# Performance work log

Measured on AMD Instinct MI355X. Metric: run time of the kernel, lower is better.

Reference implementation:

```python
import math
import jax, jax.numpy as jnp
import numpy as np

IN_DIM = 128
OUT_DIM = 128
D_TIME = 64
N_SRC = 50000
N_DST = 50000
E = 800000
SCALE = math.sqrt(2 * OUT_DIM + D_TIME)  # sqrt(attn_input_dim)


def setup_inputs() -> dict:
    key = jax.random.key(0)
    k1, k2, k3, k4, k5, k6, k7 = jax.random.split(key, 7)
    h_src = jax.random.normal(k1, (N_SRC, IN_DIM), dtype=jnp.float32)
    h_dst = jax.random.normal(k2, (N_DST, IN_DIM), dtype=jnp.float32)
    edge_index = jax.random.randint(k3, (2, E), 0, N_DST, dtype=jnp.int32)
    phi_dt = jax.random.normal(k4, (E, D_TIME), dtype=jnp.float32)
    # parameters (Kaiming-ish scaling like nn.Linear defaults)
    W_src = jax.random.normal(k5, (OUT_DIM, IN_DIM), dtype=jnp.float32) / math.sqrt(IN_DIM)
    W_dst = jax.random.normal(k6, (OUT_DIM, IN_DIM), dtype=jnp.float32) / math.sqrt(IN_DIM)
    attn_w = jax.random.normal(k7, (2 * OUT_DIM + D_TIME,), dtype=jnp.float32) / math.sqrt(2 * OUT_DIM + D_TIME)
    return {"h_src": h_src, "h_dst": h_dst, "edge_index": edge_index,
            "phi_dt": phi_dt, "W_src": W_src, "W_dst": W_dst, "attn_w": attn_w}


def reference(h_src, h_dst, edge_index, phi_dt, W_src, W_dst, attn_w):
    num_dst = h_dst.shape[0]
    src_idx, dst_idx = edge_index[0], edge_index[1]
    # gather + per-edge linear projections: [E, out_dim]
    z_s = h_src[src_idx] @ W_src.T
    z_d = h_dst[dst_idx] @ W_dst.T
    # attn(cat([z_s, z_d, phi])) == z_s@a_s + z_d@a_d + phi@a_t (avoids concat)
    a_s = attn_w[:OUT_DIM]
    a_d = attn_w[OUT_DIM:2 * OUT_DIM]
    a_t = attn_w[2 * OUT_DIM:]
    e = z_s @ a_s + z_d @ a_d + phi_dt @ a_t  # [E]
    e = jax.nn.leaky_relu(e, 0.2) / SCALE
    # numerically stable segment softmax over dst neighbourhoods
    seg_max = jax.ops.segment_max(e, dst_idx, num_segments=num_dst)
    ex = jnp.exp(e - seg_max[dst_idx])
    seg_sum = jax.ops.segment_sum(ex, dst_idx, num_segments=num_dst)
    alpha = ex / (seg_sum[dst_idx] + 1e-12)
    # dropout is identity at inference
    msg = alpha[:, None] * z_s  # [E, out_dim]
    out = jax.ops.segment_sum(msg, dst_idx, num_segments=num_dst)  # [N_dst, out_dim]
    return out
```

## Files before the change

### kernel.cpp

```cpp
#include <hip/hip_runtime.h>
#include <hip/hip_fp16.h>
#include <math.h>

#define IN_DIM   128
#define OUT_DIM  128
#define D_TIME   64
#define NSRC     50000
#define NDST     50000
#define NE       800000
#define NPB      20
#define SLOTS    64
#define EPB      256
#define INV_SCALE 0.05590169943749474f

__global__ __launch_bounds__(256) void k_prevec(const float* __restrict__ Ws,
                                                const float* __restrict__ Wd,
                                                const float* __restrict__ attn,
                                                float* __restrict__ v_s,
                                                float* __restrict__ v_d){
    int wv = threadIdx.x >> 6, lane = threadIdx.x & 63;
    int o = blockIdx.x * 4 + wv;
    const float* W = (o < 128) ? Ws : Wd;
    const float* a = (o < 128) ? attn : attn + OUT_DIM;
    float*       v = (o < 128) ? v_s : v_d;
    int k = o & 127;
    int j = 2 * lane;
    float acc = W[(size_t)j*IN_DIM + k] * a[j] + W[(size_t)(j+1)*IN_DIM + k] * a[j+1];
    #pragma unroll
    for (int off = 32; off > 0; off >>= 1) acc += __shfl_down(acc, off, 64);
    if (lane == 0) v[k] = acc;
}

__global__ __launch_bounds__(256, 4) void k_front(const float* __restrict__ h_src,
                                                  const float* __restrict__ h_dst,
                                                  const float* __restrict__ W,
                                                  const float* __restrict__ v_s,
                                                  const float* __restrict__ v_d,
                                                  __half* __restrict__ Zh,
                                                  float* __restrict__ s_src,
                                                  float* __restrict__ s_dst,
                                                  int* __restrict__ counts){
    int t = threadIdx.x;
    if (blockIdx.x < NSRC/NPB){
        __shared__ float hbuf[2][IN_DIM];
        int r  = t >> 1;
        int kh = t & 1;
        float4 wreg[16];
        const float4* wvp = (const float4*)(W + (size_t)r * IN_DIM + kh * 64);
        #pragma unroll
        for (int i = 0; i < 16; ++i) wreg[i] = wvp[i];
        int base = blockIdx.x * NPB;
        if (t < IN_DIM) hbuf[0][t] = h_src[(size_t)base*IN_DIM + t];
        for (int nn = 0; nn < NPB; ++nn){
            __syncthreads();
            if (nn + 1 < NPB && t < IN_DIM)
                hbuf[(nn+1)&1][t] = h_src[(size_t)(base+nn+1)*IN_DIM + t];
            const float* hc = hbuf[nn&1] + kh*64;
            float acc = 0.f;
            #pragma unroll
            for (int i = 0; i < 16; ++i){
                float4 w = wreg[i]; int k = i*4;
                acc += hc[k+0]*w.x + hc[k+1]*w.y + hc[k+2]*w.z + hc[k+3]*w.w;
            }
            acc += __shfl_xor(acc, 1, 64);
            if (!kh) Zh[(size_t)(base+nn)*OUT_DIM + r] = __float2half_rn(acc);
        }
    } else {
        __shared__ float vd[IN_DIM];
        int b = blockIdx.x - NSRC/NPB;
        bool isDst = (b >= NSRC/4);
        const float* h = isDst ? h_dst : h_src;
        const float* v = isDst ? v_d  : v_s;
        float*       s = isDst ? s_dst : s_src;
        int bb = isDst ? (b - NSRC/4) : b;
        if (t < IN_DIM) vd[t] = v[t];
        __syncthreads();
        int wave = t >> 6, lane = t & 63;
        int node = bb * 4 + wave;
        float2 u = ((const float2*)(h + (size_t)node*IN_DIM))[lane];
        float acc = u.x*vd[2*lane] + u.y*vd[2*lane+1];
        #pragma unroll
        for (int off = 32; off > 0; off >>= 1) acc += __shfl_down(acc, off, 64);
        if (lane == 0){
            s[node] = acc;
            if (isDst) counts[node] = 0;
        }
    }
}

__global__ __launch_bounds__(256) void k_edge(const float* __restrict__ phi,
                                              const float* __restrict__ attn,
                                              const int* __restrict__ ei,
                                              const float* __restrict__ s_src,
                                              const float* __restrict__ s_dst,
                                              int2* __restrict__ slots,
                                              int* __restrict__ counts){
    __shared__ float at[D_TIME];
    __shared__ float pts[EPB];
    int t = threadIdx.x;
    if (t < D_TIME) at[t] = attn[2*OUT_DIM + t];
    __syncthreads();
    int sub = t & 15, g = t >> 4;
    int e0 = blockIdx.x * EPB + g;
    float a0 = at[sub*4+0], a1 = at[sub*4+1], a2 = at[sub*4+2], a3 = at[sub*4+3];
    #pragma unroll
    for (int pp = 0; pp < 16; pp += 4){
        float4 w[4];
        #pragma unroll
        for (int q = 0; q < 4; ++q)
            w[q] = ((const float4*)(phi + (size_t)(e0 + (pp+q)*16) * D_TIME))[sub];
        #pragma unroll
        for (int q = 0; q < 4; ++q){
            float acc = w[q].x*a0 + w[q].y*a1 + w[q].z*a2 + w[q].w*a3;
            #pragma unroll
            for (int off = 8; off > 0; off >>= 1) acc += __shfl_xor(acc, off, 64);
            if (sub == 0) pts[g + (pp+q)*16] = acc;
        }
    }
    __syncthreads();
    int e = blockIdx.x * EPB + t;
    int src = ei[e], dst = ei[NE + e];
    float v = s_src[src] + s_dst[dst] + pts[t];
    v = (v > 0.f) ? v : 0.2f * v;
    v *= INV_SCALE;
    int k = atomicAdd(&counts[dst], 1);
    if (k < SLOTS) slots[(dst << 6) + k] = make_int2(src, __float_as_int(v));
}

__global__ __launch_bounds__(256) void k_agg(const int* __restrict__ counts,
                                             const int2* __restrict__ slots,
                                             const __half* __restrict__ Zh,
                                             float* __restrict__ out){
    int wv = threadIdx.x >> 6, lane = threadIdx.x & 63;
    int d = blockIdx.x * 4 + wv;
    int cnt = counts[d]; cnt = (cnt > SLOTS) ? SLOTS : cnt;
    float e = -1e30f; int src = 0;
    if (lane < cnt){
        int2 s = slots[(d << 6) + lane];
        src = s.x; e = __int_as_float(s.y);
    }
    float m = e;
    #pragma unroll
    for (int off = 32; off > 0; off >>= 1) m = fmaxf(m, __shfl_xor(m, off, 64));
    float ex = (lane < cnt) ? __expf(e - m) : 0.f;
    float sum = ex;
    #pragma unroll
    for (int off = 32; off > 0; off >>= 1) sum += __shfl_xor(sum, off, 64);
    float alpha = ex / (sum + 1e-12f);
    float2 acc = make_float2(0.f, 0.f);
    int jmax = (cnt + 7) & ~7;
    for (int j = 0; j < jmax; j += 8){
        float a[8]; int s[8];
        #pragma unroll
        for (int q = 0; q < 8; ++q){
            a[q] = __shfl(alpha, j+q, 64);
            s[q] = __shfl(src,   j+q, 64);
        }
        __half2 z[8];
        #pragma unroll
        for (int q = 0; q < 8; ++q)
            z[q] = ((const __half2*)(Zh + (size_t)s[q] * OUT_DIM))[lane];
        #pragma unroll
        for (int q = 0; q < 8; ++q){
            float2 f = __half22float2(z[q]);
            acc.x += a[q]*f.x;
            acc.y += a[q]*f.y;
        }
    }
    ((float2*)(out + (size_t)d * OUT_DIM))[lane] = acc;
}

extern "C" void kernel_launch(void* const* d_in, const int* in_sizes, int n_in,
                              void* d_out, int out_size, void* d_ws, size_t ws_size,
                              hipStream_t stream){
    const float* h_src = (const float*)d_in[0];
    const float* h_dst = (const float*)d_in[1];
    const int*   ei    = (const int*)d_in[2];
    const float* phi   = (const float*)d_in[3];
    const float* Wsrc  = (const float*)d_in[4];
    const float* Wdst  = (const float*)d_in[5];
    const float* attn  = (const float*)d_in[6];
    float* out = (float*)d_out;

    char* p = (char*)d_ws;
    auto alloc = [&](size_t bytes)->char*{
        char* r = p; p += (bytes + 255) / 256 * 256; return r;
    };
    __half* Zh   = (__half*)alloc((size_t)NSRC*OUT_DIM*2);
    float* s_src = (float*)alloc((size_t)NSRC*4);
    float* s_dst = (float*)alloc((size_t)NDST*4);
    float* v_s   = (float*)alloc(128*4);
    float* v_d   = (float*)alloc(128*4);
    int2*  slots = (int2*)alloc((size_t)NDST*SLOTS*8);
    int*   counts= (int*)alloc((size_t)NDST*4);

    k_prevec<<<64, 256, 0, stream>>>(Wsrc, Wdst, attn, v_s, v_d);
    k_front<<<NSRC/NPB + (NSRC + NDST)/4, 256, 0, stream>>>(
        h_src, h_dst, Wsrc, v_s, v_d, Zh, s_src, s_dst, counts);
    k_edge<<<NE/EPB, 256, 0, stream>>>(phi, attn, ei, s_src, s_dst, slots, counts);
    k_agg<<<NDST/4, 256, 0, stream>>>(counts, slots, Zh, out);
}
```

Before: 463.3 us.

## Fuse src score into projection, batch rows, widen gathers in aggregation

Computes s_src directly from the projected Z rows inside the src projection blocks, so the separate h_src reread and v_s precompute are dropped. The projection now processes four rows per sync round with 40 nodes per block, and dst scoring handles 16 nodes per block. The edge kernel issues 8 phi loads at a time, and aggregation has each half-wave gather different edges with 8-byte loads, then combines the halves with a shuffle. This trades extra shuffle reductions and register pressure for less redundant memory traffic and fewer barriers.

```diff
diff --git a/kernel.cpp b/kernel.cpp
--- a/kernel.cpp
+++ b/kernel.cpp
@@ -8,33 +8,31 @@
 #define NSRC     50000
 #define NDST     50000
 #define NE       800000
-#define NPB      20
+#define NPB      40
+#define GR       4
+#define NR       (NPB/GR)
+#define DPB      16
 #define SLOTS    64
 #define EPB      256
 #define INV_SCALE 0.05590169943749474f
 
-__global__ __launch_bounds__(256) void k_prevec(const float* __restrict__ Ws,
-                                                const float* __restrict__ Wd,
+__global__ __launch_bounds__(256) void k_prevec(const float* __restrict__ Wd,
                                                 const float* __restrict__ attn,
-                                                float* __restrict__ v_s,
                                                 float* __restrict__ v_d){
     int wv = threadIdx.x >> 6, lane = threadIdx.x & 63;
-    int o = blockIdx.x * 4 + wv;
-    const float* W = (o < 128) ? Ws : Wd;
-    const float* a = (o < 128) ? attn : attn + OUT_DIM;
-    float*       v = (o < 128) ? v_s : v_d;
-    int k = o & 127;
+    int k = blockIdx.x * 4 + wv;
     int j = 2 * lane;
-    float acc = W[(size_t)j*IN_DIM + k] * a[j] + W[(size_t)(j+1)*IN_DIM + k] * a[j+1];
+    float acc = Wd[(size_t)j*IN_DIM + k] * attn[OUT_DIM + j]
+              + Wd[(size_t)(j+1)*IN_DIM + k] * attn[OUT_DIM + j + 1];
     #pragma unroll
     for (int off = 32; off > 0; off >>= 1) acc += __shfl_down(acc, off, 64);
-    if (lane == 0) v[k] = acc;
+    if (lane == 0) v_d[k] = acc;
 }
 
 __global__ __launch_bounds__(256, 4) void k_front(const float* __restrict__ h_src,
                                                   const float* __restrict__ h_dst,
                                                   const float* __restrict__ W,
-                                                  const float* __restrict__ v_s,
+                                                  const float* __restrict__ attn,
                                                   const float* __restrict__ v_d,
                                                   __half* __restrict__ Zh,
                                                   float* __restrict__ s_src,
@@ -42,48 +40,73 @@
                                                   int* __restrict__ counts){
     int t = threadIdx.x;
     if (blockIdx.x < NSRC/NPB){
-        __shared__ float hbuf[2][IN_DIM];
+        __shared__ float hbuf[2][GR][IN_DIM];
+        __shared__ float sred[2][4][GR];
         int r  = t >> 1;
         int kh = t & 1;
+        int wv = t >> 6, lane = t & 63;
+        float a_r = attn[r];
         float4 wreg[16];
         const float4* wvp = (const float4*)(W + (size_t)r * IN_DIM + kh * 64);
         #pragma unroll
         for (int i = 0; i < 16; ++i) wreg[i] = wvp[i];
         int base = blockIdx.x * NPB;
-        if (t < IN_DIM) hbuf[0][t] = h_src[(size_t)base*IN_DIM + t];
-        for (int nn = 0; nn < NPB; ++nn){
+        ((float2*)hbuf[0][wv])[lane] =
+            ((const float2*)(h_src + (size_t)(base + wv)*IN_DIM))[lane];
+        for (int rnd = 0; rnd < NR; ++rnd){
             __syncthreads();
-            if (nn + 1 < NPB && t < IN_DIM)
-                hbuf[(nn+1)&1][t] = h_src[(size_t)(base+nn+1)*IN_DIM + t];
-            const float* hc = hbuf[nn&1] + kh*64;
-            float acc = 0.f;
+            if (rnd + 1 < NR)
+                ((float2*)hbuf[(rnd+1)&1][wv])[lane] =
+                    ((const float2*)(h_src + (size_t)(base + (rnd+1)*GR + wv)*IN_DIM))[lane];
+            if (rnd > 0 && t < GR){
+                int pb = (rnd-1)&1;
+                s_src[base + (rnd-1)*GR + t] =
+                    0.5f*(sred[pb][0][t]+sred[pb][1][t]+sred[pb][2][t]+sred[pb][3][t]);
+            }
             #pragma unroll
-            for (int i = 0; i < 16; ++i){
-                float4 w = wreg[i]; int k = i*4;
-                acc += hc[k+0]*w.x + hc[k+1]*w.y + hc[k+2]*w.z + hc[k+3]*w.w;
+            for (int g = 0; g < GR; ++g){
+                const float* hc = hbuf[rnd&1][g] + kh*64;
+                float acc = 0.f;
+                #pragma unroll
+                for (int i = 0; i < 16; ++i){
+                    float4 w = wreg[i]; int k = i*4;
+                    acc += hc[k+0]*w.x + hc[k+1]*w.y + hc[k+2]*w.z + hc[k+3]*w.w;
+                }
+                acc += __shfl_xor(acc, 1, 64);
+                if (!kh) Zh[(size_t)(base+rnd*GR+g)*OUT_DIM + r] = __float2half_rn(acc);
+                float c = acc * a_r;
+                #pragma unroll
+                for (int off = 32; off > 0; off >>= 1) c += __shfl_xor(c, off, 64);
+                if (lane == 0) sred[rnd&1][wv][g] = c;
             }
-            acc += __shfl_xor(acc, 1, 64);
-            if (!kh) Zh[(size_t)(base+nn)*OUT_DIM + r] = __float2half_rn(acc);
+        }
+        __syncthreads();
+        if (t < GR){
+            int pb = (NR-1)&1;
+            s_src[base + (NR-1)*GR + t] =
+                0.5f*(sred[pb][0][t]+sred[pb][1][t]+sred[pb][2][t]+sred[pb][3][t]);
         }
     } else {
         __shared__ float vd[IN_DIM];
         int b = blockIdx.x - NSRC/NPB;
-        bool isDst = (b >= NSRC/4);
-        const float* h = isDst ? h_dst : h_src;
-        const float* v = isDst ? v_d  : v_s;
-        float*       s = isDst ? s_dst : s_src;
-        int bb = isDst ? (b - NSRC/4) : b;
-        if (t < IN_DIM) vd[t] = v[t];
+        if (t < IN_DIM) vd[t] = v_d[t];
         __syncthreads();
-        int wave = t >> 6, lane = t & 63;
-        int node = bb * 4 + wave;
-        float2 u = ((const float2*)(h + (size_t)node*IN_DIM))[lane];
-        float acc = u.x*vd[2*lane] + u.y*vd[2*lane+1];
-        #pragma unroll
-        for (int off = 32; off > 0; off >>= 1) acc += __shfl_down(acc, off, 64);
-        if (lane == 0){
-            s[node] = acc;
-            if (isDst) counts[node] = 0;
+        int wv = t >> 6, lane = t & 63;
+        float v0 = vd[2*lane], v1 = vd[2*lane+1];
+        int n0 = b * DPB + wv;
+        float2 u[4];
+        #pragma unroll
+        for (int it = 0; it < 4; ++it)
+            u[it] = ((const float2*)(h_dst + (size_t)(n0 + it*4)*IN_DIM))[lane];
+        #pragma unroll
+        for (int it = 0; it < 4; ++it){
+            float acc = u[it].x*v0 + u[it].y*v1;
+            #pragma unroll
+            for (int off = 32; off > 0; off >>= 1) acc += __shfl_down(acc, off, 64);
+            if (lane == 0){
+                s_dst[n0 + it*4] = acc;
+                counts[n0 + it*4] = 0;
+            }
         }
     }
 }
@@ -104,13 +127,13 @@
     int e0 = blockIdx.x * EPB + g;
     float a0 = at[sub*4+0], a1 = at[sub*4+1], a2 = at[sub*4+2], a3 = at[sub*4+3];
     #pragma unroll
-    for (int pp = 0; pp < 16; pp += 4){
-        float4 w[4];
-        #pragma unroll
-        for (int q = 0; q < 4; ++q)
+    for (int pp = 0; pp < 16; pp += 8){
+        float4 w[8];
+        #pragma unroll
+        for (int q = 0; q < 8; ++q)
             w[q] = ((const float4*)(phi + (size_t)(e0 + (pp+q)*16) * D_TIME))[sub];
         #pragma unroll
-        for (int q = 0; q < 4; ++q){
+        for (int q = 0; q < 8; ++q){
             float acc = w[q].x*a0 + w[q].y*a1 + w[q].z*a2 + w[q].w*a3;
             #pragma unroll
             for (int off = 8; off > 0; off >>= 1) acc += __shfl_xor(acc, off, 64);
@@ -132,6 +155,7 @@
                                              const __half* __restrict__ Zh,
                                              float* __restrict__ out){
     int wv = threadIdx.x >> 6, lane = threadIdx.x & 63;
+    int half = lane >> 5, sl = lane & 31;
     int d = blockIdx.x * 4 + wv;
     int cnt = counts[d]; cnt = (cnt > SLOTS) ? SLOTS : cnt;
     float e = -1e30f; int src = 0;
@@ -147,27 +171,35 @@
     #pragma unroll
     for (int off = 32; off > 0; off >>= 1) sum += __shfl_xor(sum, off, 64);
     float alpha = ex / (sum + 1e-12f);
-    float2 acc = make_float2(0.f, 0.f);
+    float4 acc4 = make_float4(0.f, 0.f, 0.f, 0.f);
     int jmax = (cnt + 7) & ~7;
     for (int j = 0; j < jmax; j += 8){
-        float a[8]; int s[8];
-        #pragma unroll
-        for (int q = 0; q < 8; ++q){
-            a[q] = __shfl(alpha, j+q, 64);
-            s[q] = __shfl(src,   j+q, 64);
-        }
-        __half2 z[8];
-        #pragma unroll
-        for (int q = 0; q < 8; ++q)
-            z[q] = ((const __half2*)(Zh + (size_t)s[q] * OUT_DIM))[lane];
-        #pragma unroll
-        for (int q = 0; q < 8; ++q){
-            float2 f = __half22float2(z[q]);
-            acc.x += a[q]*f.x;
-            acc.y += a[q]*f.y;
-        }
-    }
-    ((float2*)(out + (size_t)d * OUT_DIM))[lane] = acc;
+        float a[4]; int s[4];
+        #pragma unroll
+        for (int q = 0; q < 4; ++q){
+            int idx = j + 2*q + half;
+            a[q] = __shfl(alpha, idx, 64);
+            s[q] = __shfl(src,   idx, 64);
+        }
+        float2 raw[4];
+        #pragma unroll
+        for (int q = 0; q < 4; ++q)
+            raw[q] = ((const float2*)(Zh + (size_t)s[q] * OUT_DIM))[sl];
+        #pragma unroll
+        for (int q = 0; q < 4; ++q){
+            __half2 h0 = *(__half2*)&raw[q].x;
+            __half2 h1 = *(__half2*)&raw[q].y;
+            float2 f0 = __half22float2(h0);
+            float2 f1 = __half22float2(h1);
+            acc4.x += a[q]*f0.x; acc4.y += a[q]*f0.y;
+            acc4.z += a[q]*f1.x; acc4.w += a[q]*f1.y;
+        }
+    }
+    acc4.x += __shfl_xor(acc4.x, 32, 64);
+    acc4.y += __shfl_xor(acc4.y, 32, 64);
+    acc4.z += __shfl_xor(acc4.z, 32, 64);
+    acc4.w += __shfl_xor(acc4.w, 32, 64);
+    if (!half) ((float4*)(out + (size_t)d * OUT_DIM))[sl] = acc4;
 }
 
 extern "C" void kernel_launch(void* const* d_in, const int* in_sizes, int n_in,
@@ -189,14 +221,13 @@
     __half* Zh   = (__half*)alloc((size_t)NSRC*OUT_DIM*2);
     float* s_src = (float*)alloc((size_t)NSRC*4);
     float* s_dst = (float*)alloc((size_t)NDST*4);
-    float* v_s   = (float*)alloc(128*4);
     float* v_d   = (float*)alloc(128*4);
     int2*  slots = (int2*)alloc((size_t)NDST*SLOTS*8);
     int*   counts= (int*)alloc((size_t)NDST*4);
 
-    k_prevec<<<64, 256, 0, stream>>>(Wsrc, Wdst, attn, v_s, v_d);
-    k_front<<<NSRC/NPB + (NSRC + NDST)/4, 256, 0, stream>>>(
-        h_src, h_dst, Wsrc, v_s, v_d, Zh, s_src, s_dst, counts);
+    k_prevec<<<32, 256, 0, stream>>>(Wdst, attn, v_d);
+    k_front<<<NSRC/NPB + NDST/DPB, 256, 0, stream>>>(
+        h_src, h_dst, Wsrc, attn, v_d, Zh, s_src, s_dst, counts);
     k_edge<<<NE/EPB, 256, 0, stream>>>(phi, attn, ei, s_src, s_dst, slots, counts);
     k_agg<<<NDST/4, 256, 0, stream>>>(counts, slots, Zh, out);
 }
```

Result: faster. 449.7 us (-2.9%).
